# Optimization experiments

Hardware: AMD Instinct MI355X
Metric: run time of the kernel (lower is better)

## Reference

```python
import jax, jax.numpy as jnp
import numpy as np

B, S, D_MODEL, H, BLOCK = 2, 4096, 1024, 16, 512
HEAD = D_MODEL // H  # 64


def setup_inputs() -> dict:
    key = jax.random.key(0)
    ks = jax.random.split(key, 5)
    w_scale = 1.0 / np.sqrt(D_MODEL)  # variance_scaling(1.0,'fan_in','normal')-like magnitude
    return {
        "inputs_q": jax.random.normal(ks[0], (B, S, D_MODEL), jnp.float32),
        "Wq": jax.random.normal(ks[1], (D_MODEL, D_MODEL), jnp.float32) * w_scale,
        "bq": jnp.zeros((D_MODEL,), jnp.float32),
        "Wk": jax.random.normal(ks[2], (D_MODEL, D_MODEL), jnp.float32) * w_scale,
        "bk": jnp.zeros((D_MODEL,), jnp.float32),
        "Wv": jax.random.normal(ks[3], (D_MODEL, D_MODEL), jnp.float32) * w_scale,
        "bv": jnp.zeros((D_MODEL,), jnp.float32),
        "Wo": jax.random.normal(ks[4], (D_MODEL, D_MODEL), jnp.float32) * w_scale,
        "bo": jnp.zeros((D_MODEL,), jnp.float32),
    }


def _flash_attention(q, k, v):
    """Blocked online-softmax attention. q,k,v: [B,S,H,D] -> [B,S,H,D].

    Scans over KV blocks of size BLOCK, maintaining running max (m),
    running sum of exp (l), and unnormalized output (o), exactly matching
    the original module's blocked accumulation math (no mask/bias/dropout).
    """
    scale = 1.0 / jnp.sqrt(jnp.asarray(HEAD, q.dtype))
    n_kv_blocks = S // BLOCK
    # [n_blocks, B, BLOCK, H, D]
    kb = k.reshape(B, n_kv_blocks, BLOCK, H, HEAD).transpose(1, 0, 2, 3, 4)
    vb = v.reshape(B, n_kv_blocks, BLOCK, H, HEAD).transpose(1, 0, 2, 3, 4)

    o0 = jnp.zeros_like(q)                                   # [B,S,H,D]
    m0 = jnp.full((B, S, H), -jnp.inf, dtype=q.dtype)        # running max
    l0 = jnp.zeros((B, S, H), dtype=q.dtype)                 # running sum-exp

    def step(carry, kv):
        o, m, l = carry
        k_blk, v_blk = kv
        # [B,H,S,BLOCK] scores for all queries vs this kv block
        scores = jnp.einsum('bqhd,bkhd->bhqk', q, k_blk) * scale
        blk_max = jnp.max(scores, axis=-1).transpose(0, 2, 1)   # [B,S,H]
        new_m = jnp.maximum(m, blk_max)
        alpha = jnp.exp(m - new_m)                               # rescale old stats
        p = jnp.exp(scores - new_m.transpose(0, 2, 1)[..., None])
        new_l = alpha * l + jnp.sum(p, axis=-1).transpose(0, 2, 1)
        new_o = o * alpha[..., None] + jnp.einsum('bhqk,bkhd->bqhd', p, v_blk)
        return (new_o, new_m, new_l), None

    (o, m, l), _ = jax.lax.scan(step, (o0, m0, l0), (kb, vb))
    return o / l[..., None]


def reference(inputs_q, Wq, bq, Wk, bk, Wv, bv, Wo, bo):
    q = (inputs_q @ Wq + bq).reshape(B, S, H, HEAD)
    k = (inputs_q @ Wk + bk).reshape(B, S, H, HEAD)  # self-attention: k=v=q input
    v = (inputs_q @ Wv + bv).reshape(B, S, H, HEAD)
    x = _flash_attention(q, k, v).reshape(B, S, D_MODEL)
    return x @ Wo + bo
```

## Files before the change

### kernel.cpp

```cpp
#include <hip/hip_runtime.h>
#include <hip/hip_bf16.h>
#include <stdint.h>

#define B_ 2
#define S_ 4096
#define DM 1024
#define H_ 16
#define HD 64
#define M_TOT (B_*S_)

typedef unsigned short u16;
typedef short s16x8 __attribute__((ext_vector_type(8)));
typedef short s16x4 __attribute__((ext_vector_type(4)));
typedef float f32x4 __attribute__((ext_vector_type(4)));
typedef uint32_t u32x2 __attribute__((ext_vector_type(2)));

#if __has_builtin(__builtin_amdgcn_mfma_f32_16x16x16_bf16)
#define MFMA16(A,B,C) __builtin_amdgcn_mfma_f32_16x16x16_bf16(A,B,C,0,0,0)
#elif __has_builtin(__builtin_amdgcn_mfma_f32_16x16x16bf16_1k)
#define MFMA16(A,B,C) __builtin_amdgcn_mfma_f32_16x16x16bf16_1k(A,B,C,0,0,0)
#else
static __device__ __forceinline__ f32x4 mfma16_asm(s16x4 a, s16x4 b, f32x4 c){
  f32x4 d;
  asm volatile("v_mfma_f32_16x16x16_bf16 %0, %1, %2, %3" : "=v"(d) : "v"(a), "v"(b), "v"(c));
  return d;
}
#define MFMA16(A,B,C) mfma16_asm(A,B,C)
#endif

__device__ __forceinline__ u16 f2bf(float f){
  union { float fv; uint32_t u; } x; x.fv = f;
  uint32_t r = (x.u + 0x7fffu + ((x.u >> 16) & 1u)) >> 16;
  return (u16)r;
}

#if __has_builtin(__builtin_amdgcn_cvt_pk_bf16_f32)
typedef __bf16 bf16x2_t __attribute__((ext_vector_type(2)));
__device__ __forceinline__ uint32_t pkbf(float a, float b){
  union { bf16x2_t v; uint32_t u; } x;
  x.v = __builtin_amdgcn_cvt_pk_bf16_f32(a, b);
  return x.u;
}
#else
__device__ __forceinline__ uint32_t pkbf(float a, float b){
  union { float f; uint32_t u; } xa, xb; xa.f = a; xb.f = b;
  return __builtin_amdgcn_perm(xb.u + 0x8000u, xa.u + 0x8000u, 0x07060302u);
}
#endif

__device__ __forceinline__ void gld_lds16(const void* g, void* l){
  __builtin_amdgcn_global_load_lds((const __attribute__((address_space(1))) void*)g,
                                   (__attribute__((address_space(3))) void*)l, 16, 0, 0);
}

__global__ __launch_bounds__(256) void k_cvt_x(const float* __restrict__ x, u16* __restrict__ xb){
  size_t i = (size_t)blockIdx.x * 256 + threadIdx.x;
  const float4* p = (const float4*)x + i*2;
  float4 a = p[0], b = p[1];
  union { u16 u[8]; uint4 v; } o;
  o.u[0]=f2bf(a.x); o.u[1]=f2bf(a.y); o.u[2]=f2bf(a.z); o.u[3]=f2bf(a.w);
  o.u[4]=f2bf(b.x); o.u[5]=f2bf(b.y); o.u[6]=f2bf(b.z); o.u[7]=f2bf(b.w);
  ((uint4*)xb)[i] = o.v;
}

__global__ __launch_bounds__(256) void k_wt(const float* __restrict__ W0, const float* __restrict__ W1,
                                            const float* __restrict__ W2, const float* __restrict__ W3,
                                            u16* __restrict__ wt){
  const float* W = blockIdx.z==0?W0: blockIdx.z==1?W1: blockIdx.z==2?W2:W3;
  u16* out = wt + (size_t)blockIdx.z * DM * DM;
  int n0 = blockIdx.x*64, k0 = blockIdx.y*64;
  __shared__ u16 T[64*66];
  int t = threadIdx.x;
  #pragma unroll
  for (int i=0;i<4;i++){
    int idx = t + i*256;
    int kr = idx >> 4, n4 = idx & 15;
    float4 v = *(const float4*)(W + (size_t)(k0+kr)*DM + n0 + n4*4);
    T[(n4*4+0)*66 + kr] = f2bf(v.x);
    T[(n4*4+1)*66 + kr] = f2bf(v.y);
    T[(n4*4+2)*66 + kr] = f2bf(v.z);
    T[(n4*4+3)*66 + kr] = f2bf(v.w);
  }
  __syncthreads();
  #pragma unroll
  for (int i=0;i<2;i++){
    int idx = t + i*256;
    int n = idx >> 3, k8 = idx & 7;
    union { u16 u[8]; uint4 v; } o;
    #pragma unroll
    for (int j=0;j<8;j++) o.u[j] = T[n*66 + k8*8 + j];
    *(uint4*)(out + (size_t)(n0+n)*DM + k0 + k8*8) = o.v;
  }
}

__device__ __forceinline__ void gemm128(const u16* __restrict__ A, const u16* __restrict__ BT,
                                        const float* __restrict__ bias, bool brow, float scale,
                                        u16* __restrict__ outb, float* __restrict__ outf,
                                        int m0, int n0, int ldo){
  __shared__ __align__(16) u16 As[128*64];
  __shared__ __align__(16) u16 Bs[128*64];
  int t = threadIdx.x;
  int lane = t & 63, w = t >> 6;
  int wm = w & 1, wn = w >> 1;
  int c16 = lane & 15, quad = lane >> 4;
  f32x4 acc[4][4] = {};
  const u16* ap[4]; const u16* bp[4];
  #pragma unroll
  for (int i=0;i<4;i++){
    int c = t + i*256;
    int row = c >> 3, scol = (c & 7) ^ (row & 7);
    ap[i] = A  + (size_t)(m0+row)*DM + scol*8;
    bp[i] = BT + (size_t)(n0+row)*DM + scol*8;
  }
  for (int k0 = 0; k0 < DM; k0 += 64){
    #pragma unroll
    for (int i=0;i<4;i++){
      int c = t + i*256;
      gld_lds16(ap[i] + k0, &As[c*8]);
      gld_lds16(bp[i] + k0, &Bs[c*8]);
    }
    __syncthreads();
    #pragma unroll
    for (int ks=0; ks<2; ks++){
      s16x8 af[4], bfr[4];
      #pragma unroll
      for (int mi=0;mi<4;mi++){
        int row = wm*64 + mi*16 + c16;
        af[mi] = *(const s16x8*)&As[row*64 + (((ks*4 + quad) ^ (row & 7))*8)];
      }
      #pragma unroll
      for (int ni=0;ni<4;ni++){
        int row = wn*64 + ni*16 + c16;
        bfr[ni] = *(const s16x8*)&Bs[row*64 + (((ks*4 + quad) ^ (row & 7))*8)];
      }
      #pragma unroll
      for (int mi=0;mi<4;mi++)
        #pragma unroll
        for (int ni=0;ni<4;ni++)
          acc[mi][ni] = __builtin_amdgcn_mfma_f32_16x16x32_bf16(af[mi], bfr[ni], acc[mi][ni], 0, 0, 0);
    }
    __syncthreads();
  }
  #pragma unroll
  for (int mi=0;mi<4;mi++){
    #pragma unroll
    for (int ni=0;ni<4;ni++){
      int col = n0 + wn*64 + ni*16 + c16;
      float bc = brow ? 0.0f : bias[col];
      #pragma unroll
      for (int r=0;r<4;r++){
        int row = m0 + wm*64 + mi*16 + quad*4 + r;
        float bb = brow ? bias[row] : bc;
        float v = (acc[mi][ni][r] + bb) * scale;
        if (outb) outb[(size_t)row*ldo + col] = f2bf(v);
        else      outf[(size_t)row*ldo + col] = v;
      }
    }
  }
}

#define CL2 0.18033688011112042f

__device__ __forceinline__ void gemm_swz(int wg, int& m0, int& n0){
  int xcd = wg & 7, loc = wg >> 3;
  m0 = ((xcd << 3) + (loc >> 3)) * 128;
  n0 = (loc & 7) * 128;
}

__global__ __launch_bounds__(256) void k_gemm_qkv(const u16* __restrict__ xb, const u16* __restrict__ wt,
                                                  const float* __restrict__ b0, const float* __restrict__ b1,
                                                  const float* __restrict__ b2,
                                                  u16* __restrict__ q, u16* __restrict__ k, u16* __restrict__ vt){
  int z = blockIdx.z;
  int m0, n0;
  gemm_swz(blockIdx.x + (blockIdx.y << 3), m0, n0);
  const u16* Aarg; const u16* Barg; const float* bias; float scale; u16* out;
  int mm, nn, ldo; bool brow;
  if (z == 2){
    Aarg = wt + 2*(size_t)DM*DM; Barg = xb; bias = b2; brow = true;  scale = 1.0f;
    out = vt; mm = n0; nn = m0; ldo = M_TOT;
  } else {
    Aarg = xb; Barg = wt + (size_t)z*DM*DM; bias = z ? b1 : b0; brow = false;
    scale = z ? 1.0f : CL2; out = z ? k : q; mm = m0; nn = n0; ldo = DM;
  }
  gemm128(Aarg, Barg, bias, brow, scale, out, nullptr, mm, nn, ldo);
}

__global__ __launch_bounds__(256) void k_gemm_out(const u16* __restrict__ ab, const u16* __restrict__ wto,
                                                  const float* __restrict__ bias, float* __restrict__ out){
  int m0, n0;
  gemm_swz(blockIdx.x + (blockIdx.y << 3), m0, n0);
  gemm128(ab, wto, bias, false, 1.0f, nullptr, out, m0, n0, DM);
}

__global__ __launch_bounds__(512, 2) void k_attn(const u16* __restrict__ qg, const u16* __restrict__ kg,
                                                 const u16* __restrict__ vtg, u16* __restrict__ ao){
  __shared__ __align__(16) char smem[67584];
  float* Ob  = (float*)smem;
  u16*   ObT = (u16*)smem;
  float* Lb  = (float*)(smem + 65536);

  int t = threadIdx.x, lane = t & 63, w = t >> 6;
  int c16 = lane & 15, quad = lane >> 4;
  int qq = w & 3, kh = w >> 2;
  int wg = blockIdx.x + (blockIdx.y << 4) + (blockIdx.z << 8);
  int xcd = wg & 7, loc = wg >> 3;
  int nw = (xcd << 6) + loc;
  int q0 = (nw & 15) * 256;
  int hb = nw >> 4;
  int h = hb & 15, b = hb >> 4;
  size_t rowbase = (size_t)b * S_;
  const u16* vbase = vtg + ((size_t)h*64)*M_TOT + b*S_;

  int krow0 = t >> 3,         ksw0 = ((t & 7) ^ (krow0 & 7));
  int krow1 = (t + 512) >> 3, ksw1 = ((t & 7) ^ (krow1 & 7));
  const u16* kgp0 = kg + (rowbase + krow0)*DM + h*64 + ksw0*8;
  const u16* kgp1 = kg + (rowbase + krow1)*DM + h*64 + ksw1*8;
  int vrow0 = t >> 4,         vsw0 = ((t & 15) ^ (vrow0 & 15));
  int vrow1 = (t + 512) >> 4, vsw1 = ((t & 15) ^ (vrow1 & 15));
  const u16* vgp0 = vbase + (size_t)vrow0*M_TOT + vsw0*8;
  const u16* vgp1 = vbase + (size_t)vrow1*M_TOT + vsw1*8;
  char* kd0 = smem + t*16;
  char* kd1 = smem + t*16 + 8192;
  char* vd0 = smem + 16384 + t*16;
  char* vd1 = smem + 16384 + t*16 + 8192;

  auto stage = [&](int boff, int kv0){
    size_t ko = (size_t)kv0 * DM;
    gld_lds16(kgp0 + ko, kd0 + boff);
    gld_lds16(kgp1 + ko, kd1 + boff);
    gld_lds16(vgp0 + kv0, vd0 + boff);
    gld_lds16(vgp1 + kv0, vd1 + boff);
  };

  stage(0, 0);

  s16x8 qf[4][2];
  #pragma unroll
  for (int nt=0;nt<4;nt++)
    #pragma unroll
    for (int ks=0;ks<2;ks++)
      qf[nt][ks] = *(const s16x8*)(qg + (rowbase + q0 + qq*64 + nt*16 + c16)*DM + h*64 + ks*32 + quad*8);

  f32x4 oacc[4][4] = {};
  float lacc[4] = {0.f,0.f,0.f,0.f};

  auto compute = [&](int boff){
    const u16* Kt = (const u16*)(smem + boff);
    const u16* Vt = (const u16*)(smem + boff + 16384);

    f32x4 sc[4][4] = {};
    #pragma unroll
    for (int mt=0;mt<4;mt++){
      #pragma unroll
      for (int ks=0;ks<2;ks++){
        s16x8 kf = *(const s16x8*)&Kt[(kh*64 + mt*16 + c16)*64 + (((ks*4 + quad) ^ (c16 & 7)) * 8)];
        #pragma unroll
        for (int nt=0;nt<4;nt++)
          sc[mt][nt] = __builtin_amdgcn_mfma_f32_16x16x32_bf16(kf, qf[nt][ks], sc[mt][nt], 0,0,0);
      }
    }

    uint32_t pk[4][4][2];
    #pragma unroll
    for (int mt=0;mt<4;mt++){
      #pragma unroll
      for (int nt=0;nt<4;nt++){
        float p0 = __builtin_amdgcn_exp2f(sc[mt][nt][0]);
        float p1 = __builtin_amdgcn_exp2f(sc[mt][nt][1]);
        float p2 = __builtin_amdgcn_exp2f(sc[mt][nt][2]);
        float p3 = __builtin_amdgcn_exp2f(sc[mt][nt][3]);
        lacc[nt] += (p0 + p1) + (p2 + p3);
        pk[mt][nt][0] = pkbf(p0, p1);
        pk[mt][nt][1] = pkbf(p2, p3);
      }
    }

    #pragma unroll
    for (int mt=0;mt<4;mt++){
      #pragma unroll
      for (int dt=0;dt<4;dt++){
        s16x4 vf = *(const s16x4*)&Vt[(dt*16 + c16)*128 + (((kh*8 + mt*2 + (quad>>1)) ^ c16) * 8) + (quad & 1)*4];
        #pragma unroll
        for (int nt=0;nt<4;nt++){
          union { uint32_t u[2]; s16x4 v; } pp;
          pp.u[0] = pk[mt][nt][0]; pp.u[1] = pk[mt][nt][1];
          oacc[dt][nt] = MFMA16(vf, pp.v, oacc[dt][nt]);
        }
      }
    }
  };

  #define NT (S_/128)
  #pragma unroll 1
  for (int kvt = 0; kvt < NT-1; ++kvt){
    stage(((kvt+1) & 1) * 32768, (kvt+1)*128);
    asm volatile("s_waitcnt vmcnt(4)" ::: "memory");
    __builtin_amdgcn_s_barrier();
    __builtin_amdgcn_sched_barrier(0);
    compute((kvt & 1) * 32768);
    __builtin_amdgcn_s_barrier();
    __builtin_amdgcn_sched_barrier(0);
  }
  asm volatile("s_waitcnt vmcnt(0)" ::: "memory");
  __builtin_amdgcn_s_barrier();
  __builtin_amdgcn_sched_barrier(0);
  compute(((NT-1) & 1) * 32768);

  float lw[4];
  #pragma unroll
  for (int nt=0;nt<4;nt++){
    float l = lacc[nt];
    l += __shfl_xor(l, 16);
    l += __shfl_xor(l, 32);
    lw[nt] = l;
  }
  __syncthreads();
  if (quad == 0){
    #pragma unroll
    for (int nt=0;nt<4;nt++) Lb[kh*256 + qq*64 + nt*16 + c16] = lw[nt];
  }
  uint32_t pko[4][4][2];
  float invl[4];
  #pragma unroll
  for (int dh=0; dh<2; dh++){
    if (kh == 1){
      #pragma unroll
      for (int dt2=0;dt2<2;dt2++)
        #pragma unroll
        for (int nt=0;nt<4;nt++)
          *(f32x4*)&Ob[(qq*64 + nt*16 + c16)*36 + dt2*16 + quad*4] = oacc[dh*2+dt2][nt];
    }
    __syncthreads();
    if (kh == 0){
      if (dh == 0){
        #pragma unroll
        for (int nt=0;nt<4;nt++){
          int ql = qq*64 + nt*16 + c16;
          invl[nt] = 1.0f / (Lb[ql] + Lb[256 + ql]);
        }
      }
      #pragma unroll
      for (int dt2=0;dt2<2;dt2++)
        #pragma unroll
        for (int nt=0;nt<4;nt++){
          f32x4 p = *(const f32x4*)&Ob[(qq*64 + nt*16 + c16)*36 + dt2*16 + quad*4];
          f32x4 o = oacc[dh*2+dt2][nt] + p;
          pko[dh*2+dt2][nt][0] = pkbf(o[0]*invl[nt], o[1]*invl[nt]);
          pko[dh*2+dt2][nt][1] = pkbf(o[2]*invl[nt], o[3]*invl[nt]);
        }
    }
    __syncthreads();
  }
  if (kh == 0){
    #pragma unroll
    for (int dt=0;dt<4;dt++)
      #pragma unroll
      for (int nt=0;nt<4;nt++){
        u32x2 pr; pr.x = pko[dt][nt][0]; pr.y = pko[dt][nt][1];
        *(u32x2*)&ObT[(qq*64 + nt*16 + c16)*72 + dt*16 + quad*4] = pr;
      }
  }
  __syncthreads();
  #pragma unroll
  for (int i=0;i<4;i++){
    int idx = t + i*512;
    int qr = idx >> 3, qc = (idx & 7)*8;
    *(s16x8*)(ao + (rowbase + q0 + qr)*DM + h*64 + qc) = *(const s16x8*)&ObT[qr*72 + qc];
  }
}

extern "C" void kernel_launch(void* const* d_in, const int* in_sizes, int n_in,
                              void* d_out, int out_size, void* d_ws, size_t ws_size,
                              hipStream_t stream){
  const float* x  = (const float*)d_in[0];
  const float* Wq = (const float*)d_in[1];
  const float* bq = (const float*)d_in[2];
  const float* Wk = (const float*)d_in[3];
  const float* bk = (const float*)d_in[4];
  const float* Wv = (const float*)d_in[5];
  const float* bv = (const float*)d_in[6];
  const float* Wo = (const float*)d_in[7];
  const float* bo = (const float*)d_in[8];

  char* ws = (char*)d_ws;
  const size_t XB = (size_t)M_TOT*DM*2;
  const size_t WTB = (size_t)4*DM*DM*2;
  u16* xb  = (u16*)(ws);
  u16* wt  = (u16*)(ws + XB);
  u16* qb  = (u16*)(ws + XB + WTB);
  u16* kb  = (u16*)(ws + XB + WTB + XB);
  u16* vtb = (u16*)(ws + XB + WTB + 2*XB);
  u16* aob = (u16*)(ws + XB + WTB + 3*XB);

  k_cvt_x<<<dim3((M_TOT*DM)/(256*8)), 256, 0, stream>>>(x, xb);
  k_wt<<<dim3(16,16,4), 256, 0, stream>>>(Wq, Wk, Wv, Wo, wt);
  k_gemm_qkv<<<dim3(8, M_TOT/128, 3), 256, 0, stream>>>(xb, wt, bq, bk, bv, qb, kb, vtb);
  k_attn<<<dim3(S_/256, H_, B_), 512, 0, stream>>>(qb, kb, vtb, aob);
  k_gemm_out<<<dim3(8, M_TOT/128), 256, 0, stream>>>(aob, wt + (size_t)3*DM*DM, bo, (float*)d_out);
}
```

Baseline: 349.3 us.

## Merge prep kernels, shrink GEMM k-tile, use K=32 MFMA in attention PV

Merges the input-conversion and weight-transpose kernels into one launch to save a kernel launch. Changes the projection GEMM to a 32-wide k-tile with no XOR swizzle, halving LDS per block but doubling the number of barriers and likely adding LDS bank conflicts. In attention, pairs adjacent P/V sub-tiles so the PV product uses the 16x16x32 bf16 MFMA instead of two 16x16x16 ones, halving the MFMA instruction count.

```diff
diff --git a/kernel.cpp b/kernel.cpp
--- a/kernel.cpp
+++ b/kernel.cpp
@@ -15,19 +15,6 @@
 typedef float f32x4 __attribute__((ext_vector_type(4)));
 typedef uint32_t u32x2 __attribute__((ext_vector_type(2)));
 
-#if __has_builtin(__builtin_amdgcn_mfma_f32_16x16x16_bf16)
-#define MFMA16(A,B,C) __builtin_amdgcn_mfma_f32_16x16x16_bf16(A,B,C,0,0,0)
-#elif __has_builtin(__builtin_amdgcn_mfma_f32_16x16x16bf16_1k)
-#define MFMA16(A,B,C) __builtin_amdgcn_mfma_f32_16x16x16bf16_1k(A,B,C,0,0,0)
-#else
-static __device__ __forceinline__ f32x4 mfma16_asm(s16x4 a, s16x4 b, f32x4 c){
-  f32x4 d;
-  asm volatile("v_mfma_f32_16x16x16_bf16 %0, %1, %2, %3" : "=v"(d) : "v"(a), "v"(b), "v"(c));
-  return d;
-}
-#define MFMA16(A,B,C) mfma16_asm(A,B,C)
-#endif
-
 __device__ __forceinline__ u16 f2bf(float f){
   union { float fv; uint32_t u; } x; x.fv = f;
   uint32_t r = (x.u + 0x7fffu + ((x.u >> 16) & 1u)) >> 16;
@@ -53,28 +40,31 @@
                                    (__attribute__((address_space(3))) void*)l, 16, 0, 0);
 }
 
-__global__ __launch_bounds__(256) void k_cvt_x(const float* __restrict__ x, u16* __restrict__ xb){
-  size_t i = (size_t)blockIdx.x * 256 + threadIdx.x;
-  const float4* p = (const float4*)x + i*2;
-  float4 a = p[0], b = p[1];
-  union { u16 u[8]; uint4 v; } o;
-  o.u[0]=f2bf(a.x); o.u[1]=f2bf(a.y); o.u[2]=f2bf(a.z); o.u[3]=f2bf(a.w);
-  o.u[4]=f2bf(b.x); o.u[5]=f2bf(b.y); o.u[6]=f2bf(b.z); o.u[7]=f2bf(b.w);
-  ((uint4*)xb)[i] = o.v;
-}
-
-__global__ __launch_bounds__(256) void k_wt(const float* __restrict__ W0, const float* __restrict__ W1,
-                                            const float* __restrict__ W2, const float* __restrict__ W3,
-                                            u16* __restrict__ wt){
-  const float* W = blockIdx.z==0?W0: blockIdx.z==1?W1: blockIdx.z==2?W2:W3;
-  u16* out = wt + (size_t)blockIdx.z * DM * DM;
-  int n0 = blockIdx.x*64, k0 = blockIdx.y*64;
+__global__ __launch_bounds__(256) void k_prep(const float* __restrict__ x, u16* __restrict__ xb,
+                                              const float* __restrict__ W0, const float* __restrict__ W1,
+                                              const float* __restrict__ W2, const float* __restrict__ W3,
+                                              u16* __restrict__ wt){
   __shared__ u16 T[64*66];
   int t = threadIdx.x;
+  if (blockIdx.x < 4096){
+    size_t i = (size_t)blockIdx.x * 256 + t;
+    const float4* p = (const float4*)x + i*2;
+    float4 a = p[0], b = p[1];
+    union { u16 u[8]; uint4 v; } o;
+    o.u[0]=f2bf(a.x); o.u[1]=f2bf(a.y); o.u[2]=f2bf(a.z); o.u[3]=f2bf(a.w);
+    o.u[4]=f2bf(b.x); o.u[5]=f2bf(b.y); o.u[6]=f2bf(b.z); o.u[7]=f2bf(b.w);
+    ((uint4*)xb)[i] = o.v;
+    return;
+  }
+  int idx = blockIdx.x - 4096;
+  int bx = idx & 15, by = (idx >> 4) & 15, bz = idx >> 8;
+  const float* W = bz==0?W0: bz==1?W1: bz==2?W2:W3;
+  u16* out = wt + (size_t)bz * DM * DM;
+  int n0 = bx*64, k0 = by*64;
   #pragma unroll
   for (int i=0;i<4;i++){
-    int idx = t + i*256;
-    int kr = idx >> 4, n4 = idx & 15;
+    int id2 = t + i*256;
+    int kr = id2 >> 4, n4 = id2 & 15;
     float4 v = *(const float4*)(W + (size_t)(k0+kr)*DM + n0 + n4*4);
     T[(n4*4+0)*66 + kr] = f2bf(v.x);
     T[(n4*4+1)*66 + kr] = f2bf(v.y);
@@ -84,8 +74,8 @@
   __syncthreads();
   #pragma unroll
   for (int i=0;i<2;i++){
-    int idx = t + i*256;
-    int n = idx >> 3, k8 = idx & 7;
+    int id2 = t + i*256;
+    int n = id2 >> 3, k8 = id2 & 7;
     union { u16 u[8]; uint4 v; } o;
     #pragma unroll
     for (int j=0;j<8;j++) o.u[j] = T[n*66 + k8*8 + j];
@@ -97,48 +87,32 @@
                                         const float* __restrict__ bias, bool brow, float scale,
                                         u16* __restrict__ outb, float* __restrict__ outf,
                                         int m0, int n0, int ldo){
-  __shared__ __align__(16) u16 As[128*64];
-  __shared__ __align__(16) u16 Bs[128*64];
+  __shared__ __align__(16) u16 As[128*32];
+  __shared__ __align__(16) u16 Bs[128*32];
   int t = threadIdx.x;
   int lane = t & 63, w = t >> 6;
   int wm = w & 1, wn = w >> 1;
   int c16 = lane & 15, quad = lane >> 4;
   f32x4 acc[4][4] = {};
-  const u16* ap[4]; const u16* bp[4];
-  #pragma unroll
-  for (int i=0;i<4;i++){
-    int c = t + i*256;
-    int row = c >> 3, scol = (c & 7) ^ (row & 7);
-    ap[i] = A  + (size_t)(m0+row)*DM + scol*8;
-    bp[i] = BT + (size_t)(n0+row)*DM + scol*8;
-  }
-  for (int k0 = 0; k0 < DM; k0 += 64){
-    #pragma unroll
-    for (int i=0;i<4;i++){
-      int c = t + i*256;
-      gld_lds16(ap[i] + k0, &As[c*8]);
-      gld_lds16(bp[i] + k0, &Bs[c*8]);
+  for (int k0 = 0; k0 < DM; k0 += 32){
+    #pragma unroll
+    for (int i=0;i<2;i++){
+      int idx = t + i*256;
+      int row = idx >> 2, c8 = (idx & 3) << 3;
+      gld_lds16(A  + (size_t)(m0+row)*DM + k0 + c8, &As[idx*8]);
+      gld_lds16(BT + (size_t)(n0+row)*DM + k0 + c8, &Bs[idx*8]);
     }
     __syncthreads();
-    #pragma unroll
-    for (int ks=0; ks<2; ks++){
-      s16x8 af[4], bfr[4];
-      #pragma unroll
-      for (int mi=0;mi<4;mi++){
-        int row = wm*64 + mi*16 + c16;
-        af[mi] = *(const s16x8*)&As[row*64 + (((ks*4 + quad) ^ (row & 7))*8)];
-      }
-      #pragma unroll
-      for (int ni=0;ni<4;ni++){
-        int row = wn*64 + ni*16 + c16;
-        bfr[ni] = *(const s16x8*)&Bs[row*64 + (((ks*4 + quad) ^ (row & 7))*8)];
-      }
-      #pragma unroll
-      for (int mi=0;mi<4;mi++)
-        #pragma unroll
-        for (int ni=0;ni<4;ni++)
-          acc[mi][ni] = __builtin_amdgcn_mfma_f32_16x16x32_bf16(af[mi], bfr[ni], acc[mi][ni], 0, 0, 0);
-    }
+    s16x8 af[4], bf[4];
+    #pragma unroll
+    for (int mi=0;mi<4;mi++) af[mi] = *(const s16x8*)&As[(wm*64+mi*16+c16)*32 + quad*8];
+    #pragma unroll
+    for (int ni=0;ni<4;ni++) bf[ni] = *(const s16x8*)&Bs[(wn*64+ni*16+c16)*32 + quad*8];
+    #pragma unroll
+    for (int mi=0;mi<4;mi++)
+      #pragma unroll
+      for (int ni=0;ni<4;ni++)
+        acc[mi][ni] = __builtin_amdgcn_mfma_f32_16x16x32_bf16(af[mi], bf[ni], acc[mi][ni], 0, 0, 0);
     __syncthreads();
   }
   #pragma unroll
@@ -174,16 +148,13 @@
   int z = blockIdx.z;
   int m0, n0;
   gemm_swz(blockIdx.x + (blockIdx.y << 3), m0, n0);
-  const u16* Aarg; const u16* Barg; const float* bias; float scale; u16* out;
-  int mm, nn, ldo; bool brow;
   if (z == 2){
-    Aarg = wt + 2*(size_t)DM*DM; Barg = xb; bias = b2; brow = true;  scale = 1.0f;
-    out = vt; mm = n0; nn = m0; ldo = M_TOT;
+    gemm128(wt + 2*(size_t)DM*DM, xb, b2, true, 1.0f, vt, nullptr,
+            n0, m0, M_TOT);
   } else {
-    Aarg = xb; Barg = wt + (size_t)z*DM*DM; bias = z ? b1 : b0; brow = false;
-    scale = z ? 1.0f : CL2; out = z ? k : q; mm = m0; nn = n0; ldo = DM;
-  }
-  gemm128(Aarg, Barg, bias, brow, scale, out, nullptr, mm, nn, ldo);
+    gemm128(xb, wt + (size_t)z*DM*DM, z ? b1 : b0, false, z ? 1.0f : CL2,
+            z ? k : q, nullptr, m0, n0, DM);
+  }
 }
 
 __global__ __launch_bounds__(256) void k_gemm_out(const u16* __restrict__ ab, const u16* __restrict__ wto,
@@ -277,15 +248,19 @@
     }
 
     #pragma unroll
-    for (int mt=0;mt<4;mt++){
+    for (int mp=0;mp<2;mp++){
+      int mtA = mp*2, mtB = mp*2+1;
       #pragma unroll
       for (int dt=0;dt<4;dt++){
-        s16x4 vf = *(const s16x4*)&Vt[(dt*16 + c16)*128 + (((kh*8 + mt*2 + (quad>>1)) ^ c16) * 8) + (quad & 1)*4];
+        union { s16x4 h[2]; s16x8 v8; } vf;
+        vf.h[0] = *(const s16x4*)&Vt[(dt*16 + c16)*128 + (((kh*8 + mtA*2 + (quad>>1)) ^ c16) * 8) + (quad & 1)*4];
+        vf.h[1] = *(const s16x4*)&Vt[(dt*16 + c16)*128 + (((kh*8 + mtB*2 + (quad>>1)) ^ c16) * 8) + (quad & 1)*4];
         #pragma unroll
         for (int nt=0;nt<4;nt++){
-          union { uint32_t u[2]; s16x4 v; } pp;
-          pp.u[0] = pk[mt][nt][0]; pp.u[1] = pk[mt][nt][1];
-          oacc[dt][nt] = MFMA16(vf, pp.v, oacc[dt][nt]);
+          union { uint32_t u[4]; s16x8 v; } pp;
+          pp.u[0] = pk[mtA][nt][0]; pp.u[1] = pk[mtA][nt][1];
+          pp.u[2] = pk[mtB][nt][0]; pp.u[3] = pk[mtB][nt][1];
+          oacc[dt][nt] = __builtin_amdgcn_mfma_f32_16x16x32_bf16(vf.v8, pp.v, oacc[dt][nt], 0,0,0);
         }
       }
     }
@@ -393,8 +368,7 @@
   u16* vtb = (u16*)(ws + XB + WTB + 2*XB);
   u16* aob = (u16*)(ws + XB + WTB + 3*XB);
 
-  k_cvt_x<<<dim3((M_TOT*DM)/(256*8)), 256, 0, stream>>>(x, xb);
-  k_wt<<<dim3(16,16,4), 256, 0, stream>>>(Wq, Wk, Wv, Wo, wt);
+  k_prep<<<dim3(4096 + 1024), 256, 0, stream>>>(x, xb, Wq, Wk, Wv, Wo, wt);
   k_gemm_qkv<<<dim3(8, M_TOT/128, 3), 256, 0, stream>>>(xb, wt, bq, bk, bv, qb, kb, vtb);
   k_attn<<<dim3(S_/256, H_, B_), 512, 0, stream>>>(qb, kb, vtb, aob);
   k_gemm_out<<<dim3(8, M_TOT/128), 256, 0, stream>>>(aob, wt + (size_t)3*DM*DM, bo, (float*)d_out);
```

After: 344.1 us, median of 2. Within noise of the previous version (-1.5%).
